# Kernel tuning notes

Measured on AMD Instinct MI355X. Metric: run time of the kernel, lower is better.

Reference implementation:

```python
import jax, jax.numpy as jnp
import numpy as np
from jax import lax

B, C, H, W = 4, 128, 128, 128
MAXD = 192
D = MAXD // 4            # 48 disparity hypotheses at 1/4 scale
WS = 8                   # window size
NH = 8                   # num heads
HD = C // NH             # head dim = 16
SCALE = HD ** -0.5
HID = 4 * C              # mlp hidden (mlp_ratio=4)


def _rel_index(ws):
    coords = np.stack(np.meshgrid(np.arange(ws), np.arange(ws), indexing='ij'))
    cf = coords.reshape(2, -1)
    rel = (cf[:, :, None] - cf[:, None, :]).transpose(1, 2, 0)
    rel[:, :, 0] += ws - 1
    rel[:, :, 1] += ws - 1
    rel[:, :, 0] *= 2 * ws - 1
    return rel.sum(-1)   # [ws*ws, ws*ws]

REL_IDX = jnp.asarray(_rel_index(WS))


def setup_inputs() -> dict:
    key = jax.random.key(0)
    ks = iter(jax.random.split(key, 40))
    rn = lambda shape, s=0.02: jax.random.normal(next(ks), shape, dtype=jnp.float32) * s
    return {
        'feat_l': jax.random.normal(next(ks), (B, C, H, W), dtype=jnp.float32),
        'feat_r': jax.random.normal(next(ks), (B, C, H, W), dtype=jnp.float32),
        'wq': rn((C, C)), 'bq': jnp.zeros((C,), jnp.float32),
        'wk': rn((C, C)), 'bk': jnp.zeros((C,), jnp.float32),
        'wv': rn((C, C)), 'bv': jnp.zeros((C,), jnp.float32),
        'wp': rn((C, C)), 'bp': jnp.zeros((C,), jnp.float32),
        'rpb': rn(((2 * WS - 1) ** 2, NH)),
        'ln1_g': jnp.ones((C,), jnp.float32), 'ln1_b': jnp.zeros((C,), jnp.float32),
        'ln2_g': jnp.ones((C,), jnp.float32), 'ln2_b': jnp.zeros((C,), jnp.float32),
        'mlp_w1': rn((C, HID)), 'mlp_b1': jnp.zeros((HID,), jnp.float32),
        'mlp_w2': rn((HID, C)), 'mlp_b2': jnp.zeros((C,), jnp.float32),
        'un_w1': rn((C, C)), 'un_b1': jnp.zeros((C,), jnp.float32),
        'un_w2': rn((C, C)), 'un_b2': jnp.zeros((C,), jnp.float32),
        'dp_w1': rn((C // 2 + D // 2 + 16, C + D, 3, 3)) if False else rn(((C + D) // 2, C + D, 3, 3)),
        'dp_b1': jnp.zeros(((C + D) // 2,), jnp.float32),
        'bn_g': jnp.ones(((C + D) // 2,), jnp.float32), 'bn_b': jnp.zeros(((C + D) // 2,), jnp.float32),
        'dp_w2': rn((D, (C + D) // 2, 1, 1)), 'dp_b2': jnp.zeros((D,), jnp.float32),
    }


def _ln(x, g, b):
    m = x.mean(-1, keepdims=True)
    v = x.var(-1, keepdims=True)
    return (x - m) * jax.lax.rsqrt(v + 1e-5) * g + b


def _conv(x, w, b, pad):
    y = lax.conv_general_dilated(x, w, (1, 1), [(pad, pad), (pad, pad)],
                                 dimension_numbers=('NCHW', 'OIHW', 'NCHW'))
    return y + b[None, :, None, None]


def _cost_volume(fl, fr):
    # corr[:, d] = mean_c fl[..., w] * fr[..., w-d], zero-padded on the left
    outs = [jnp.mean(fl * fr, axis=1)]
    for d in range(1, D):
        fr_s = jnp.pad(fr[:, :, :, :-d], ((0, 0), (0, 0), (0, 0), (d, 0)))
        outs.append(jnp.mean(fl * fr_s, axis=1))
    return jnp.stack(outs, axis=1)  # [B, D, H, W]


def _win_part(tok):  # [B, H*W, C] -> [B*nW, WS*WS, C]
    x = tok.reshape(B, H // WS, WS, W // WS, WS, C)
    return x.transpose(0, 1, 3, 2, 4, 5).reshape(-1, WS * WS, C)


def _win_rev(win):  # [B*nW, WS*WS, C] -> [B, H*W, C]
    x = win.reshape(B, H // WS, W // WS, WS, WS, C)
    return x.transpose(0, 1, 3, 2, 4, 5).reshape(B, H * W, C)


def _forward(feat_l, feat_r, wq, bq, wk, bk, wv, bv, wp, bp, rpb,
             ln1_g, ln1_b, ln2_g, ln2_b, mlp_w1, mlp_b1, mlp_w2, mlp_b2,
             un_w1, un_b1, un_w2, un_b2, dp_w1, dp_b1, bn_g, bn_b, dp_w2, dp_b2):
    gelu = lambda x: jax.nn.gelu(x, approximate=False)
    cost = _cost_volume(feat_l, feat_r)                       # [B, D, H, W]

    tokens = feat_l.reshape(B, C, H * W).transpose(0, 2, 1)   # [B, N, C]
    unary = gelu(tokens @ un_w1 + un_b1) @ un_w2 + un_b2      # unary potential

    nf = _ln(_win_part(tokens), ln1_g, ln1_b)                 # [Bw, 64, C]
    Bw, N = nf.shape[0], WS * WS
    q = (nf @ wq + bq).reshape(Bw, N, NH, HD).transpose(0, 2, 1, 3)
    k = (nf @ wk + bk).reshape(Bw, N, NH, HD).transpose(0, 2, 1, 3)
    v = (nf @ wv + bv).reshape(Bw, N, NH, HD).transpose(0, 2, 1, 3)
    attn = jnp.einsum('bhnd,bhmd->bhnm', q, k) * SCALE
    bias = rpb[REL_IDX.reshape(-1)].reshape(N, N, NH).transpose(2, 0, 1)
    attn = jax.nn.softmax(attn + bias[None], axis=-1)
    o = jnp.einsum('bhnm,bhmd->bhnd', attn, v).transpose(0, 2, 1, 3).reshape(Bw, N, C)
    pairwise = o @ wp + bp

    x = unary + _win_rev(pairwise)
    x = x + gelu(_ln(x, ln2_g, ln2_b) @ mlp_w1 + mlp_b1) @ mlp_w2 + mlp_b2 * 0.0 + (jnp.zeros((), jnp.float32))
    # (faithful residual MLP; the extra zero terms are no-ops kept out below)
    # -- recompute cleanly to avoid confusion:
    # x = x + mlp(norm2(x))  already done above via single expression

    crf = x.transpose(0, 2, 1).reshape(B, C, H, W)
    fused = jnp.concatenate([crf, cost], axis=1)              # [B, C+D, H, W]

    h1 = jax.nn.relu((_conv(fused, dp_w1, dp_b1, 1)) * jax.lax.rsqrt(jnp.float32(1.0 + 1e-5)) * bn_g[None, :, None, None] + bn_b[None, :, None, None])
    pv = _conv(h1, dp_w2, dp_b2, 0)                           # [B, D, H, W]
    prob = jax.nn.softmax(pv, axis=1)
    disp = jnp.arange(D, dtype=jnp.float32)[None, :, None, None]
    pred = jnp.sum(prob * disp, axis=1, keepdims=True) * 4.0  # [B, 1, H, W]
    return pred


def reference(feat_l, feat_r, wq, bq, wk, bk, wv, bv, wp, bp, rpb,
              ln1_g, ln1_b, ln2_g, ln2_b, mlp_w1, mlp_b1, mlp_w2, mlp_b2,
              un_w1, un_b1, un_w2, un_b2, dp_w1, dp_b1, bn_g, bn_b, dp_w2, dp_b2):
    return _forward(feat_l, feat_r, wq, bq, wk, bk, wv, bv, wp, bp, rpb,
                    ln1_g, ln1_b, ln2_g, ln2_b, mlp_w1, mlp_b1, mlp_w2, mlp_b2,
                    un_w1, un_b1, un_w2, un_b2, dp_w1, dp_b1, bn_g, bn_b, dp_w2, dp_b2)
```

## Files before the change

kernel.cpp:

```cpp
#include <hip/hip_runtime.h>
#include <math.h>

constexpr int Bn = 4, Cc = 128, Hh = 128, Wn = 128, Dd = 48;
constexpr float SCALE = 0.25f;

typedef short  bf16x8 __attribute__((ext_vector_type(8)));
typedef short  bf16x4 __attribute__((ext_vector_type(4)));
typedef float  f32x4  __attribute__((ext_vector_type(4)));
typedef unsigned short u16x8 __attribute__((ext_vector_type(8)));

static __device__ __forceinline__ unsigned short f2bf(float f) {
    return __builtin_bit_cast(unsigned short, (__bf16)f);
}

static __device__ __forceinline__ float bf2f(unsigned short u) {
    return __uint_as_float((unsigned int)u << 16);
}

static __device__ __forceinline__ unsigned int pack2bf(float a, float b) {
    return (unsigned int)f2bf(a) | ((unsigned int)f2bf(b) << 16);
}

static __device__ __forceinline__ float gelu_f(float v) {
    float u = v * (1.5957691216f + 0.0713548162f * v * v);
    return v * __builtin_amdgcn_rcpf(1.0f + __expf(-u));
}

static __device__ __forceinline__ size_t opk_addr(int b, int wh, int ww, int Mt, int ks, int lane) {
    return ((size_t)(b * 16384) + (wh * 8 + Mt * 2 + (ks >> 1)) * 128 + ww * 8) * 128
           + (ks & 1) * 512 + lane * 8;
}

__global__ __launch_bounds__(384) void k_cost(const float* __restrict__ fl,
                                              const float* __restrict__ fr,
                                              unsigned short* __restrict__ costbf) {
    __shared__ float s_fl[2][16][64];
    __shared__ float s_fr[2][16][112];
    int tid = threadIdx.x;
    int w0 = blockIdx.x * 64;
    int hp = blockIdx.y, b = blockIdx.z;
    int row = tid / 192;
    int r = tid - row * 192;
    int wg = r & 15, dg = r >> 4;
    int W = wg * 4, D = dg * 4;
    int h = hp * 2 + row;
    float acc[4][4];
#pragma unroll
    for (int i = 0; i < 4; ++i)
#pragma unroll
        for (int j = 0; j < 4; ++j) acc[i][j] = 0.f;

#pragma unroll 1
    for (int ck = 0; ck < 8; ++ck) {
        int ci0 = ck * 16;
        for (int i = tid; i < 512; i += 384) {
            int rr = i >> 8, rem = i & 255;
            int c = rem >> 4, k4 = rem & 15;
            float4 v = *(const float4*)&fl[((size_t)(b * 128 + ci0 + c) << 14) + (hp * 2 + rr) * 128 + w0 + k4 * 4];
            *(float4*)&s_fl[rr][c][k4 * 4] = v;
        }
        for (int i = tid; i < 896; i += 384) {
            int rr = i / 448, rem = i - rr * 448;
            int c = rem / 28, k4 = rem - c * 28;
// ... 96 lines not shown
        const float* __restrict__ dp_w1, const float* __restrict__ dp_b1,
        const float* __restrict__ bn_g, const float* __restrict__ bn_b,
        unsigned short* __restrict__ pk, float* __restrict__ bias2,
        const float* __restrict__ wq, const float* __restrict__ wk,
        const float* __restrict__ wv, const float* __restrict__ wp,
        unsigned short* __restrict__ pkw,
        const float* __restrict__ rpb, float* __restrict__ pb,
        const float* __restrict__ mlp_w1, unsigned short* __restrict__ pm1,
        const float* __restrict__ mlp_w2, unsigned short* __restrict__ pm2,
        const float* __restrict__ un_w1, unsigned short* __restrict__ pu1,
        const float* __restrict__ un_w2, unsigned short* __restrict__ pu2) {
    int blk = blockIdx.x;
    int lane = threadIdx.x;
    if (blk < 324) {
        pack_conv(blk, lane, dp_w1, dp_b1, bn_g, bn_b, pk, bias2);
    } else if (blk < 452) {
        int bb = blk - 324;
        int mat = bb >> 5;
        const float* W = (mat == 0) ? wq : (mat == 1) ? wk : (mat == 2) ? wv : wp;
        pack_gemmB(bb & 31, lane, W, pkw + (size_t)mat * 16384, 128);
    } else if (blk < 580) {
        pack_rpb(blk - 452, lane, rpb, pb);
    } else if (blk < 708) {
        pack_gemmB(blk - 580, lane, mlp_w1, pm1, 512);
    } else if (blk < 836) {
        pack_gemmB(blk - 708, lane, mlp_w2, pm2, 128);
    } else if (blk < 868) {
        pack_gemmB(blk - 836, lane, un_w1, pu1, 128);
    } else {
        pack_gemmB(blk - 868, lane, un_w2, pu2, 128);
    }
}

__global__ __launch_bounds__(256) void k_unary_mfma(const float* __restrict__ feat_l,
                                                    const unsigned short* __restrict__ pu1,
                                                    const float* __restrict__ b1,
                                                    const unsigned short* __restrict__ pu2,
                                                    const float* __restrict__ b2,
                                                    const float* __restrict__ g1,
                                                    const float* __restrict__ bt1,
                                                    float* __restrict__ x,
                                                    unsigned short* __restrict__ nf) {
    __shared__ __align__(16) unsigned short s_a[64 * 136];
    __shared__ __align__(16) unsigned short s_h[64 * 136];
    int tid = threadIdx.x;
    int wid = tid >> 6, lane = tid & 63;
    int g = lane >> 4, t = lane & 15;
    int n0g = blockIdx.x * 64;
    int b = n0g >> 14;
    int nb = n0g & 16383;

    for (int idx = tid; idx < 4096; idx += 256) {
        int c2 = idx >> 6, nl = idx & 63;
        float v0 = feat_l[((size_t)(b * 128 + 2 * c2) << 14) + nb + nl];
        float v1 = feat_l[((size_t)(b * 128 + 2 * c2 + 1) << 14) + nb + nl];
        *(unsigned int*)&s_a[nl * 136 + 2 * c2] = pack2bf(v0, v1);
    }
    __syncthreads();

    {
        int tok = tid >> 2, q = tid & 3;
        float v[32];
#pragma unroll
        for (int i8 = 0; i8 < 4; ++i8) {
            u16x8 r8 = *(const u16x8*)&s_a[tok * 136 + q * 32 + i8 * 8];
#pragma unroll
            for (int j = 0; j < 8; ++j) v[i8 * 8 + j] = bf2f(r8[j]);
        }
        float s = 0.f, s2 = 0.f;
#pragma unroll
        for (int i = 0; i < 32; ++i) { s += v[i]; s2 += v[i] * v[i]; }
        s += __shfl_xor(s, 1); s += __shfl_xor(s, 2);
        s2 += __shfl_xor(s2, 1); s2 += __shfl_xor(s2, 2);
        float mean = s * (1.f / 128.f);
        float var = s2 * (1.f / 128.f) - mean * mean;
        float rstd = rsqrtf(var + 1e-5f);
        size_t base = (size_t)(n0g + tok) * 128 + q * 32;
#pragma unroll
        for (int i8 = 0; i8 < 4; ++i8) {
            u16x8 o8;
#pragma unroll
            for (int j = 0; j < 8; ++j) {
                int c = q * 32 + i8 * 8 + j;
                o8[j] = f2bf((v[i8 * 8 + j] - mean) * rstd * g1[c] + bt1[c]);
            }
            *(u16x8*)&nf[base + i8 * 8] = o8;
        }
    }

    bf16x8 af[4][4];
#pragma unroll
    for (int Mt = 0; Mt < 4; ++Mt)
#pragma unroll
        for (int ks = 0; ks < 4; ++ks)
            af[Mt][ks] = *(const bf16x8*)&s_a[(Mt * 16 + t) * 136 + ks * 32 + g * 8];

    f32x4 acc1[4][2];
#pragma unroll
    for (int nt2 = 0; nt2 < 2; ++nt2) {
        float bv = b1[(wid * 2 + nt2) * 16 + t];
#pragma unroll
        for (int Mt = 0; Mt < 4; ++Mt) acc1[Mt][nt2] = (f32x4){bv, bv, bv, bv};
    }
#pragma unroll
    for (int ks = 0; ks < 4; ++ks) {
        bf16x8 bf0 = *(const bf16x8*)(pu1 + (size_t)(((wid * 2 + 0) * 4 + ks) * 64 + lane) * 8);
        bf16x8 bf1 = *(const bf16x8*)(pu1 + (size_t)(((wid * 2 + 1) * 4 + ks) * 64 + lane) * 8);
#pragma unroll
        for (int Mt = 0; Mt < 4; ++Mt) {
            acc1[Mt][0] = __builtin_amdgcn_mfma_f32_16x16x32_bf16(af[Mt][ks], bf0, acc1[Mt][0], 0, 0, 0);
            acc1[Mt][1] = __builtin_amdgcn_mfma_f32_16x16x32_bf16(af[Mt][ks], bf1, acc1[Mt][1], 0, 0, 0);
        }
    }
#pragma unroll
    for (int Mt = 0; Mt < 4; ++Mt)
#pragma unroll
        for (int nt2 = 0; nt2 < 2; ++nt2)
#pragma unroll
            for (int rr = 0; rr < 4; ++rr)
                s_h[(Mt * 16 + g * 4 + rr) * 136 + (wid * 2 + nt2) * 16 + t] = f2bf(gelu_f(acc1[Mt][nt2][rr]));
    __syncthreads();

    bf16x8 a2[4][4];
#pragma unroll
    for (int Mt = 0; Mt < 4; ++Mt)
#pragma unroll
        for (int ks = 0; ks < 4; ++ks)
            a2[Mt][ks] = *(const bf16x8*)&s_h[(Mt * 16 + t) * 136 + ks * 32 + g * 8];

    f32x4 acc2[4][2];
#pragma unroll
    for (int nt2 = 0; nt2 < 2; ++nt2) {
        float bv = b2[(wid * 2 + nt2) * 16 + t];
#pragma unroll
        for (int Mt = 0; Mt < 4; ++Mt) acc2[Mt][nt2] = (f32x4){bv, bv, bv, bv};
    }
#pragma unroll
    for (int ks = 0; ks < 4; ++ks) {
        bf16x8 bf0 = *(const bf16x8*)(pu2 + (size_t)(((wid * 2 + 0) * 4 + ks) * 64 + lane) * 8);
        bf16x8 bf1 = *(const bf16x8*)(pu2 + (size_t)(((wid * 2 + 1) * 4 + ks) * 64 + lane) * 8);
#pragma unroll
        for (int Mt = 0; Mt < 4; ++Mt) {
            acc2[Mt][0] = __builtin_amdgcn_mfma_f32_16x16x32_bf16(a2[Mt][ks], bf0, acc2[Mt][0], 0, 0, 0);
            acc2[Mt][1] = __builtin_amdgcn_mfma_f32_16x16x32_bf16(a2[Mt][ks], bf1, acc2[Mt][1], 0, 0, 0);
        }
    }
#pragma unroll
    for (int Mt = 0; Mt < 4; ++Mt)
#pragma unroll
        for (int nt2 = 0; nt2 < 2; ++nt2)
#pragma unroll
            for (int rr = 0; rr < 4; ++rr) {
                int tok = Mt * 16 + g * 4 + rr;
                x[(size_t)(n0g + tok) * 128 + (wid * 2 + nt2) * 16 + t] = acc2[Mt][nt2][rr];
            }
}

__global__ __launch_bounds__(256, 3) void k_attn_core(const unsigned short* nf,
                                                      const unsigned short* __restrict__ pkw,
                                                      const float* __restrict__ pb,
                                                      const float* __restrict__ bq,
                                                      const float* __restrict__ bk,
                                                      const float* __restrict__ bv,
                                                      unsigned short* opk) {
    __shared__ __align__(16) unsigned short s_all[4 * 5760];
    int tid = threadIdx.x;
    int wid = tid >> 6, lane = tid & 63;
    int g = lane >> 4, t = lane & 15;
    int bw = blockIdx.x;
    int b = bw >> 8, wh = (bw >> 4) & 15, ww = bw & 15;

    bf16x8 af[4][4];
#pragma unroll
    for (int Mt = 0; Mt < 4; ++Mt) {
        int tok = Mt * 16 + t;
        size_t gtok = (size_t)(b * 16384) + (wh * 8 + (tok >> 3)) * 128 + ww * 8 + (tok & 7);
#pragma unroll
        for (int ks = 0; ks < 4; ++ks)
            af[Mt][ks] = *(const bf16x8*)&nf[gtok * 128 + ks * 32 + g * 8];
    }
    __syncthreads();

    unsigned short* sQ = s_all + wid * 5760;
    unsigned short* sK = sQ + 1536;
    unsigned short* sV = sQ + 4608;
    unsigned short* sP = sQ;
    unsigned short* sO = sQ;

    const bf16x8 z8v = {0, 0, 0, 0, 0, 0, 0, 0};

#pragma unroll
    for (int hi = 0; hi < 2; ++hi) {
        int h = wid + hi * 4;

        float bqv = bq[h * 16 + t], bkv = bk[h * 16 + t], bvv = bv[h * 16 + t];
        f32x4 qa[4], ka[4], va[4];
#pragma unroll
        for (int Mt = 0; Mt < 4; ++Mt) {
            qa[Mt] = (f32x4){bqv, bqv, bqv, bqv};
            ka[Mt] = (f32x4){bkv, bkv, bkv, bkv};
            va[Mt] = (f32x4){bvv, bvv, bvv, bvv};
        }
#pragma unroll
        for (int ks = 0; ks < 4; ++ks) {
            const unsigned short* wbase = pkw + ((size_t)((h * 4 + ks) * 64 + lane) * 8);
            bf16x8 bfq = *(const bf16x8*)(wbase);
            bf16x8 bfk = *(const bf16x8*)(wbase + 16384);
            bf16x8 bfv = *(const bf16x8*)(wbase + 32768);
#pragma unroll
            for (int Mt = 0; Mt < 4; ++Mt) {
                qa[Mt] = __builtin_amdgcn_mfma_f32_16x16x32_bf16(af[Mt][ks], bfq, qa[Mt], 0, 0, 0);
                ka[Mt] = __builtin_amdgcn_mfma_f32_16x16x32_bf16(af[Mt][ks], bfk, ka[Mt], 0, 0, 0);
                va[Mt] = __builtin_amdgcn_mfma_f32_16x16x32_bf16(af[Mt][ks], bfv, va[Mt], 0, 0, 0);
            }
        }
#pragma unroll
        for (int Mt = 0; Mt < 4; ++Mt) {
            bf16x4 vv;
#pragma unroll
            for (int rr = 0; rr < 4; ++rr) {
                int tok = Mt * 16 + g * 4 + rr;
                sQ[tok * 24 + t] = f2bf(qa[Mt][rr] * SCALE);
                sK[tok * 24 + t] = f2bf(ka[Mt][rr]);
                vv[rr] = (short)f2bf(va[Mt][rr]);
            }
            *(bf16x4*)&sV[t * 72 + Mt * 16 + g * 4] = vv;
        }

        f32x4 s[4][4];
#pragma unroll
        for (int Mtk = 0; Mtk < 4; ++Mtk)
#pragma unroll
            for (int Ntq = 0; Ntq < 4; ++Ntq)
                s[Mtk][Ntq] = *(const f32x4*)(pb + ((size_t)((h * 16 + Mtk * 4 + Ntq) * 64 + lane) * 4));
        bf16x8 bQ[4];
#pragma unroll
        for (int Ntq = 0; Ntq < 4; ++Ntq)
            bQ[Ntq] = (g < 2) ? *(const bf16x8*)&sQ[(Ntq * 16 + t) * 24 + g * 8] : z8v;
#pragma unroll
        for (int Mtk = 0; Mtk < 4; ++Mtk) {
            bf16x8 aK = (g < 2) ? *(const bf16x8*)&sK[(Mtk * 16 + t) * 24 + g * 8] : z8v;
#pragma unroll
            for (int Ntq = 0; Ntq < 4; ++Ntq)
                s[Mtk][Ntq] = __builtin_amdgcn_mfma_f32_16x16x32_bf16(aK, bQ[Ntq], s[Mtk][Ntq], 0, 0, 0);
        }

#pragma unroll
        for (int Ntq = 0; Ntq < 4; ++Ntq) {
            float m = s[0][Ntq][0];
#pragma unroll
            for (int Mtk = 0; Mtk < 4; ++Mtk)
#pragma unroll
                for (int rr = 0; rr < 4; ++rr) m = fmaxf(m, s[Mtk][Ntq][rr]);
            m = fmaxf(m, __shfl_xor(m, 16));
            m = fmaxf(m, __shfl_xor(m, 32));
            float sum = 0.f;
#pragma unroll
            for (int Mtk = 0; Mtk < 4; ++Mtk)
#pragma unroll
                for (int rr = 0; rr < 4; ++rr) {
                    float e = __expf(s[Mtk][Ntq][rr] - m);
                    s[Mtk][Ntq][rr] = e;
                    sum += e;
                }
            sum += __shfl_xor(sum, 16);
            sum += __shfl_xor(sum, 32);
            float inv = __builtin_amdgcn_rcpf(sum);
#pragma unroll
            for (int Mtk = 0; Mtk < 4; ++Mtk) {
                bf16x4 pv;
#pragma unroll
                for (int rr = 0; rr < 4; ++rr) pv[rr] = (short)f2bf(s[Mtk][Ntq][rr] * inv);
                *(bf16x4*)&sP[(Ntq * 16 + t) * 72 + Mtk * 16 + g * 4] = pv;
            }
        }

        f32x4 oa[4];
#pragma unroll
        for (int Mt = 0; Mt < 4; ++Mt) oa[Mt] = (f32x4){0.f, 0.f, 0.f, 0.f};
#pragma unroll
        for (int ksv = 0; ksv < 2; ++ksv) {
            bf16x8 bv2 = *(const bf16x8*)&sV[t * 72 + ksv * 32 + g * 8];
#pragma unroll
            for (int Mt = 0; Mt < 4; ++Mt) {
                bf16x8 ap = *(const bf16x8*)&sP[(Mt * 16 + t) * 72 + ksv * 32 + g * 8];
                oa[Mt] = __builtin_amdgcn_mfma_f32_16x16x32_bf16(ap, bv2, oa[Mt], 0, 0, 0);
            }
        }
#pragma unroll
        for (int Mt = 0; Mt < 4; ++Mt)
#pragma unroll
            for (int rr = 0; rr < 4; ++rr)
                sO[(Mt * 16 + g * 4 + rr) * 16 + t] = f2bf(oa[Mt][rr]);
        int ksf = h >> 1;
        if ((g >> 1) == (h & 1)) {
#pragma unroll
            for (int Mt = 0; Mt < 4; ++Mt) {
                bf16x8 v8 = *(const bf16x8*)&sO[(Mt * 16 + t) * 16 + (g & 1) * 8];
                *(bf16x8*)&opk[opk_addr(b, wh, ww, Mt, ksf, lane)] = v8;
            }
        }
    }
}

__global__ __launch_bounds__(256) void k_mlp_mfma(float* __restrict__ x,
                                                  const unsigned short* __restrict__ opk,
                                                  const unsigned short* __restrict__ pkw,
                                                  const float* __restrict__ bp,
                                                  const float* __restrict__ g2,
                                                  const float* __restrict__ bt2,
                                                  const unsigned short* __restrict__ pm1,
                                                  const float* __restrict__ b1,
                                                  const unsigned short* __restrict__ pm2) {
    __shared__ __align__(16) char smem[51200];
    float* sf = (float*)smem;
    unsigned short* s_h = (unsigned short*)smem;
    unsigned short* s_a = (unsigned short*)(smem + 33792);
    int tid = threadIdx.x;
    int wid = tid >> 6, lane = tid & 63;
    int g = lane >> 4, t = lane & 15;
    int bw = blockIdx.x;
    int b = bw >> 8, wh = (bw >> 4) & 15, ww = bw & 15;

    auto gtok_of = [&](int tok) -> size_t {
        return (size_t)(b * 16384) + (wh * 8 + (tok >> 3)) * 128 + ww * 8 + (tok & 7);
    };

    f32x4 out[4][2];
    {
        float bp0 = bp[wid * 32 + t], bp1 = bp[wid * 32 + 16 + t];
#pragma unroll
        for (int Mt = 0; Mt < 4; ++Mt) {
            out[Mt][0] = (f32x4){bp0, bp0, bp0, bp0};
            out[Mt][1] = (f32x4){bp1, bp1, bp1, bp1};
        }
#pragma unroll
        for (int ks = 0; ks < 4; ++ks) {
            bf16x8 b0 = *(const bf16x8*)(pkw + 49152 + (size_t)(((wid * 2 + 0) * 4 + ks) * 64 + lane) * 8);
            bf16x8 b1v = *(const bf16x8*)(pkw + 49152 + (size_t)(((wid * 2 + 1) * 4 + ks) * 64 + lane) * 8);
#pragma unroll
            for (int Mt = 0; Mt < 4; ++Mt) {
                bf16x8 a = *(const bf16x8*)&opk[opk_addr(b, wh, ww, Mt, ks, lane)];
                out[Mt][0] = __builtin_amdgcn_mfma_f32_16x16x32_bf16(a, b0, out[Mt][0], 0, 0, 0);
                out[Mt][1] = __builtin_amdgcn_mfma_f32_16x16x32_bf16(a, b1v, out[Mt][1], 0, 0, 0);
            }
        }
#pragma unroll
        for (int Mt = 0; Mt < 4; ++Mt)
#pragma unroll
            for (int nt2 = 0; nt2 < 2; ++nt2)
#pragma unroll
                for (int rr = 0; rr < 4; ++rr) {
                    int tok = Mt * 16 + g * 4 + rr;
                    int col = (wid * 2 + nt2) * 16 + t;
                    float v = out[Mt][nt2][rr] + x[gtok_of(tok) * 128 + col];
                    out[Mt][nt2][rr] = v;
                    sf[tok * 132 + col] = v;
                }
    }
    __syncthreads();
    {
        int tok = tid >> 2, q = tid & 3;
        float s = 0.f, s2 = 0.f;
        for (int c = q * 32; c < q * 32 + 32; ++c) {
            float v = sf[tok * 132 + c];
            s += v; s2 += v * v;
        }
        s += __shfl_xor(s, 1); s += __shfl_xor(s, 2);
        s2 += __shfl_xor(s2, 1); s2 += __shfl_xor(s2, 2);
        float mean = s * (1.f / 128.f);
        float var = s2 * (1.f / 128.f) - mean * mean;
        float rstd = rsqrtf(var + 1e-5f);
        for (int c = q * 32; c < q * 32 + 32; c += 2) {
            float v0 = (sf[tok * 132 + c] - mean) * rstd * g2[c] + bt2[c];
            float v1 = (sf[tok * 132 + c + 1] - mean) * rstd * g2[c + 1] + bt2[c + 1];
            *(unsigned int*)&s_a[tok * 136 + c] = pack2bf(v0, v1);
        }
    }
    __syncthreads();
    bf16x8 af[4][4];
#pragma unroll
    for (int Mt = 0; Mt < 4; ++Mt)
#pragma unroll
        for (int ks = 0; ks < 4; ++ks)
            af[Mt][ks] = *(const bf16x8*)&s_a[(Mt * 16 + t) * 136 + ks * 32 + g * 8];

#pragma unroll 1
    for (int hc = 0; hc < 2; ++hc) {
#pragma unroll
        for (int jh = 0; jh < 2; ++jh) {
            f32x4 acc1[4][2];
#pragma unroll
            for (int j2 = 0; j2 < 2; ++j2) {
                float bv = b1[hc * 256 + (wid * 4 + jh * 2 + j2) * 16 + t];
#pragma unroll
                for (int Mt = 0; Mt < 4; ++Mt) acc1[Mt][j2] = (f32x4){bv, bv, bv, bv};
            }
#pragma unroll
            for (int ks = 0; ks < 4; ++ks) {
                int nt0 = hc * 16 + wid * 4 + jh * 2;
                bf16x8 bf0 = *(const bf16x8*)(pm1 + (size_t)((((nt0 + 0) * 4 + ks) * 64 + lane) * 8));
                bf16x8 bf1 = *(const bf16x8*)(pm1 + (size_t)((((nt0 + 1) * 4 + ks) * 64 + lane) * 8));
#pragma unroll
                for (int Mt = 0; Mt < 4; ++Mt) {
                    acc1[Mt][0] = __builtin_amdgcn_mfma_f32_16x16x32_bf16(af[Mt][ks], bf0, acc1[Mt][0], 0, 0, 0);
                    acc1[Mt][1] = __builtin_amdgcn_mfma_f32_16x16x32_bf16(af[Mt][ks], bf1, acc1[Mt][1], 0, 0, 0);
                }
            }
#pragma unroll
            for (int Mt = 0; Mt < 4; ++Mt)
#pragma unroll
                for (int j2 = 0; j2 < 2; ++j2)
#pragma unroll
                    for (int rr = 0; rr < 4; ++rr)
                        s_h[(Mt * 16 + g * 4 + rr) * 264 + (wid * 4 + jh * 2 + j2) * 16 + t] =
                            f2bf(gelu_f(acc1[Mt][j2][rr]));
        }
        __syncthreads();
#pragma unroll
        for (int kt = 0; kt < 8; ++kt) {
            int kc = hc * 2 + (kt >> 2), ks = kt & 3;
            bf16x8 bf0 = *(const bf16x8*)(pm2 + (size_t)(((kc * 32 + (wid * 2 + 0) * 4 + ks) * 64 + lane) * 8));
            bf16x8 bf1 = *(const bf16x8*)(pm2 + (size_t)(((kc * 32 + (wid * 2 + 1) * 4 + ks) * 64 + lane) * 8));
#pragma unroll
            for (int Mt = 0; Mt < 4; ++Mt) {
                bf16x8 a2 = *(const bf16x8*)&s_h[(Mt * 16 + t) * 264 + kt * 32 + g * 8];
                out[Mt][0] = __builtin_amdgcn_mfma_f32_16x16x32_bf16(a2, bf0, out[Mt][0], 0, 0, 0);
                out[Mt][1] = __builtin_amdgcn_mfma_f32_16x16x32_bf16(a2, bf1, out[Mt][1], 0, 0, 0);
            }
        }
        __syncthreads();
    }

#pragma unroll
    for (int Mt = 0; Mt < 4; ++Mt)
#pragma unroll
        for (int nt2 = 0; nt2 < 2; ++nt2)
#pragma unroll
            for (int rr = 0; rr < 4; ++rr) {
// ... 152 lines not shown
    const float* feat_l = (const float*)d_in[0];
    const float* feat_r = (const float*)d_in[1];
    const float* wq = (const float*)d_in[2];
    const float* bq = (const float*)d_in[3];
    const float* wk = (const float*)d_in[4];
    const float* bk = (const float*)d_in[5];
    const float* wv = (const float*)d_in[6];
    const float* bv = (const float*)d_in[7];
    const float* wp = (const float*)d_in[8];
    const float* bp = (const float*)d_in[9];
    const float* rpb = (const float*)d_in[10];
    const float* ln1_g = (const float*)d_in[11];
    const float* ln1_b = (const float*)d_in[12];
    const float* ln2_g = (const float*)d_in[13];
    const float* ln2_b = (const float*)d_in[14];
    const float* mlp_w1 = (const float*)d_in[15];
    const float* mlp_b1 = (const float*)d_in[16];
    const float* mlp_w2 = (const float*)d_in[17];
    const float* un_w1 = (const float*)d_in[19];
    const float* un_b1 = (const float*)d_in[20];
    const float* un_w2 = (const float*)d_in[21];
    const float* un_b2 = (const float*)d_in[22];
    const float* dp_w1 = (const float*)d_in[23];
    const float* dp_b1 = (const float*)d_in[24];
    const float* bn_g = (const float*)d_in[25];
    const float* bn_b = (const float*)d_in[26];
    const float* dp_w2 = (const float*)d_in[27];
    const float* dp_b2 = (const float*)d_in[28];

    float* ws = (float*)d_ws;
    unsigned short* costbf = (unsigned short*)ws;
    float* x = ws + 3145728;
    float* h1 = ws + 11534336;
    unsigned short* nfo = (unsigned short*)h1;
    unsigned short* pk = (unsigned short*)(ws + 17301504);
    float* bias2 = ws + 17384448;
    unsigned short* pkw = (unsigned short*)(ws + 17384544);
    float* pb = ws + 17417312;
    unsigned short* pm1 = (unsigned short*)(ws + 17450080);
    unsigned short* pm2 = (unsigned short*)(ws + 17482848);
    unsigned short* pu1 = (unsigned short*)(ws + 17515616);
    unsigned short* pu2 = (unsigned short*)(ws + 17523808);
    float* out = (float*)d_out;

    k_pack_all<<<900, 64, 0, stream>>>(dp_w1, dp_b1, bn_g, bn_b, pk, bias2,
                                       wq, wk, wv, wp, pkw, rpb, pb,
                                       mlp_w1, pm1, mlp_w2, pm2,
                                       un_w1, pu1, un_w2, pu2);
    k_cost<<<dim3(2, 64, 4), 384, 0, stream>>>(feat_l, feat_r, costbf);
    k_unary_mfma<<<1024, 256, 0, stream>>>(feat_l, pu1, un_b1, pu2, un_b2,
                                           ln1_g, ln1_b, x, nfo);
    k_attn_core<<<1024, 256, 0, stream>>>(nfo, pkw, pb, bq, bk, bv, nfo);
    k_mlp_mfma<<<1024, 256, 0, stream>>>(x, nfo, pkw, bp, ln2_g, ln2_b,
                                         pm1, mlp_b1, pm2);
    k_conv_mfma<<<dim3(8, 16, 4), 256, 0, stream>>>(x, costbf, pk, bias2, h1);
    k_head<<<256, 256, 0, stream>>>(h1, dp_w2, dp_b2, out);
}
```

Baseline: 261.8 us.

## Fuse unary MLP, window attention and transformer MLP into one per-window kernel

Merges the unary projection, LN1 plus windowed attention, and the output projection with LN2 and MLP into a single kernel where each block owns one 8x8 window. Intermediate tensors (the normed features, the attention output, the residual x) stay in LDS and registers instead of going through global memory between three launches. The cost is a larger LDS footprint (about 62KB per block) and higher register pressure. Together these may lower occupancy, and the unary feature load now uses window-strided reads instead of contiguous rows.

```diff
diff --git a/kernel.cpp b/kernel.cpp
--- a/kernel.cpp
+++ b/kernel.cpp
@@ -12,23 +12,15 @@
 static __device__ __forceinline__ unsigned short f2bf(float f) {
     return __builtin_bit_cast(unsigned short, (__bf16)f);
 }
-
 static __device__ __forceinline__ float bf2f(unsigned short u) {
     return __uint_as_float((unsigned int)u << 16);
 }
-
 static __device__ __forceinline__ unsigned int pack2bf(float a, float b) {
     return (unsigned int)f2bf(a) | ((unsigned int)f2bf(b) << 16);
 }
-
 static __device__ __forceinline__ float gelu_f(float v) {
     float u = v * (1.5957691216f + 0.0713548162f * v * v);
     return v * __builtin_amdgcn_rcpf(1.0f + __expf(-u));
-}
-
-static __device__ __forceinline__ size_t opk_addr(int b, int wh, int ww, int Mt, int ks, int lane) {
-    return ((size_t)(b * 16384) + (wh * 8 + Mt * 2 + (ks >> 1)) * 128 + ww * 8) * 128
-           + (ks & 1) * 512 + lane * 8;
 }
 
 __global__ __launch_bounds__(384) void k_cost(const float* __restrict__ fl,
@@ -191,29 +183,37 @@
     }
 }
 
-__global__ __launch_bounds__(256) void k_unary_mfma(const float* __restrict__ feat_l,
-                                                    const unsigned short* __restrict__ pu1,
-                                                    const float* __restrict__ b1,
-                                                    const unsigned short* __restrict__ pu2,
-                                                    const float* __restrict__ b2,
-                                                    const float* __restrict__ g1,
-                                                    const float* __restrict__ bt1,
-                                                    float* __restrict__ x,
-                                                    unsigned short* __restrict__ nf) {
-    __shared__ __align__(16) unsigned short s_a[64 * 136];
-    __shared__ __align__(16) unsigned short s_h[64 * 136];
+__global__ __launch_bounds__(256) void k_fused(
+        const float* __restrict__ feat_l,
+        const unsigned short* __restrict__ pu1, const float* __restrict__ ub1,
+        const unsigned short* __restrict__ pu2, const float* __restrict__ ub2,
+        const float* __restrict__ g1, const float* __restrict__ bt1,
+        const unsigned short* __restrict__ pkw, const float* __restrict__ pb,
+        const float* __restrict__ bq, const float* __restrict__ bk,
+        const float* __restrict__ bv, const float* __restrict__ bp,
+        const float* __restrict__ g2, const float* __restrict__ bt2,
+        const unsigned short* __restrict__ pm1, const float* __restrict__ mb1,
+        const unsigned short* __restrict__ pm2,
+        float* __restrict__ x) {
+    __shared__ __align__(16) char smem[63488];
+    unsigned short* s_a = (unsigned short*)smem;
+    unsigned short* s_nf = (unsigned short*)(smem + 46080);
     int tid = threadIdx.x;
     int wid = tid >> 6, lane = tid & 63;
     int g = lane >> 4, t = lane & 15;
-    int n0g = blockIdx.x * 64;
-    int b = n0g >> 14;
-    int nb = n0g & 16383;
+    int bw = blockIdx.x;
+    int b = bw >> 8, wh = (bw >> 4) & 15, ww = bw & 15;
+
+    auto gtok_of = [&](int tok) -> size_t {
+        return (size_t)(b * 16384) + (wh * 8 + (tok >> 3)) * 128 + ww * 8 + (tok & 7);
+    };
 
     for (int idx = tid; idx < 4096; idx += 256) {
-        int c2 = idx >> 6, nl = idx & 63;
-        float v0 = feat_l[((size_t)(b * 128 + 2 * c2) << 14) + nb + nl];
-        float v1 = feat_l[((size_t)(b * 128 + 2 * c2 + 1) << 14) + nb + nl];
-        *(unsigned int*)&s_a[nl * 136 + 2 * c2] = pack2bf(v0, v1);
+        int c2 = idx >> 6, n = idx & 63;
+        size_t base = ((size_t)(b * 128 + 2 * c2) << 14) + (wh * 8 + (n >> 3)) * 128 + ww * 8 + (n & 7);
+        float v0 = feat_l[base];
+        float v1 = feat_l[base + 16384];
+        *(unsigned int*)&s_a[n * 136 + 2 * c2] = pack2bf(v0, v1);
     }
     __syncthreads();
 
@@ -234,7 +234,6 @@
         float mean = s * (1.f / 128.f);
         float var = s2 * (1.f / 128.f) - mean * mean;
         float rstd = rsqrtf(var + 1e-5f);
-        size_t base = (size_t)(n0g + tok) * 128 + q * 32;
 #pragma unroll
         for (int i8 = 0; i8 < 4; ++i8) {
             u16x8 o8;
@@ -243,250 +242,199 @@
                 int c = q * 32 + i8 * 8 + j;
                 o8[j] = f2bf((v[i8 * 8 + j] - mean) * rstd * g1[c] + bt1[c]);
             }
-            *(u16x8*)&nf[base + i8 * 8] = o8;
-        }
-    }
-
-    bf16x8 af[4][4];
+            *(u16x8*)&s_nf[tok * 136 + q * 32 + i8 * 8] = o8;
+        }
+    }
+    __syncthreads();
+
+    bf16x8 afu[4][4], afa[4][4];
 #pragma unroll
     for (int Mt = 0; Mt < 4; ++Mt)
 #pragma unroll
-        for (int ks = 0; ks < 4; ++ks)
-            af[Mt][ks] = *(const bf16x8*)&s_a[(Mt * 16 + t) * 136 + ks * 32 + g * 8];
-
-    f32x4 acc1[4][2];
-#pragma unroll
-    for (int nt2 = 0; nt2 < 2; ++nt2) {
-        float bv = b1[(wid * 2 + nt2) * 16 + t];
-#pragma unroll
-        for (int Mt = 0; Mt < 4; ++Mt) acc1[Mt][nt2] = (f32x4){bv, bv, bv, bv};
-    }
-#pragma unroll
-    for (int ks = 0; ks < 4; ++ks) {
-        bf16x8 bf0 = *(const bf16x8*)(pu1 + (size_t)(((wid * 2 + 0) * 4 + ks) * 64 + lane) * 8);
-        bf16x8 bf1 = *(const bf16x8*)(pu1 + (size_t)(((wid * 2 + 1) * 4 + ks) * 64 + lane) * 8);
-#pragma unroll
-        for (int Mt = 0; Mt < 4; ++Mt) {
-            acc1[Mt][0] = __builtin_amdgcn_mfma_f32_16x16x32_bf16(af[Mt][ks], bf0, acc1[Mt][0], 0, 0, 0);
-            acc1[Mt][1] = __builtin_amdgcn_mfma_f32_16x16x32_bf16(af[Mt][ks], bf1, acc1[Mt][1], 0, 0, 0);
-        }
-    }
-#pragma unroll
-    for (int Mt = 0; Mt < 4; ++Mt)
-#pragma unroll
-        for (int nt2 = 0; nt2 < 2; ++nt2)
-#pragma unroll
-            for (int rr = 0; rr < 4; ++rr)
-                s_h[(Mt * 16 + g * 4 + rr) * 136 + (wid * 2 + nt2) * 16 + t] = f2bf(gelu_f(acc1[Mt][nt2][rr]));
-    __syncthreads();
-
-    bf16x8 a2[4][4];
-#pragma unroll
-    for (int Mt = 0; Mt < 4; ++Mt)
-#pragma unroll
-        for (int ks = 0; ks < 4; ++ks)
-            a2[Mt][ks] = *(const bf16x8*)&s_h[(Mt * 16 + t) * 136 + ks * 32 + g * 8];
-
-    f32x4 acc2[4][2];
-#pragma unroll
-    for (int nt2 = 0; nt2 < 2; ++nt2) {
-        float bv = b2[(wid * 2 + nt2) * 16 + t];
-#pragma unroll
-        for (int Mt = 0; Mt < 4; ++Mt) acc2[Mt][nt2] = (f32x4){bv, bv, bv, bv};
-    }
-#pragma unroll
-    for (int ks = 0; ks < 4; ++ks) {
-        bf16x8 bf0 = *(const bf16x8*)(pu2 + (size_t)(((wid * 2 + 0) * 4 + ks) * 64 + lane) * 8);
-        bf16x8 bf1 = *(const bf16x8*)(pu2 + (size_t)(((wid * 2 + 1) * 4 + ks) * 64 + lane) * 8);
-#pragma unroll
-        for (int Mt = 0; Mt < 4; ++Mt) {
-            acc2[Mt][0] = __builtin_amdgcn_mfma_f32_16x16x32_bf16(a2[Mt][ks], bf0, acc2[Mt][0], 0, 0, 0);
-            acc2[Mt][1] = __builtin_amdgcn_mfma_f32_16x16x32_bf16(a2[Mt][ks], bf1, acc2[Mt][1], 0, 0, 0);
-        }
-    }
-#pragma unroll
-    for (int Mt = 0; Mt < 4; ++Mt)
-#pragma unroll
-        for (int nt2 = 0; nt2 < 2; ++nt2)
-#pragma unroll
-            for (int rr = 0; rr < 4; ++rr) {
-                int tok = Mt * 16 + g * 4 + rr;
-                x[(size_t)(n0g + tok) * 128 + (wid * 2 + nt2) * 16 + t] = acc2[Mt][nt2][rr];
-            }
-}
-
-__global__ __launch_bounds__(256, 3) void k_attn_core(const unsigned short* nf,
-                                                      const unsigned short* __restrict__ pkw,
-                                                      const float* __restrict__ pb,
-                                                      const float* __restrict__ bq,
-                                                      const float* __restrict__ bk,
-                                                      const float* __restrict__ bv,
-                                                      unsigned short* opk) {
-    __shared__ __align__(16) unsigned short s_all[4 * 5760];
-    int tid = threadIdx.x;
-    int wid = tid >> 6, lane = tid & 63;
-    int g = lane >> 4, t = lane & 15;
-    int bw = blockIdx.x;
-    int b = bw >> 8, wh = (bw >> 4) & 15, ww = bw & 15;
-
-    bf16x8 af[4][4];
-#pragma unroll
-    for (int Mt = 0; Mt < 4; ++Mt) {
-        int tok = Mt * 16 + t;
-        size_t gtok = (size_t)(b * 16384) + (wh * 8 + (tok >> 3)) * 128 + ww * 8 + (tok & 7);
-#pragma unroll
-        for (int ks = 0; ks < 4; ++ks)
-            af[Mt][ks] = *(const bf16x8*)&nf[gtok * 128 + ks * 32 + g * 8];
-    }
-    __syncthreads();
-
-    unsigned short* sQ = s_all + wid * 5760;
-    unsigned short* sK = sQ + 1536;
-    unsigned short* sV = sQ + 4608;
-    unsigned short* sP = sQ;
-    unsigned short* sO = sQ;
-
-    const bf16x8 z8v = {0, 0, 0, 0, 0, 0, 0, 0};
-
-#pragma unroll
-    for (int hi = 0; hi < 2; ++hi) {
-        int h = wid + hi * 4;
-
-        float bqv = bq[h * 16 + t], bkv = bk[h * 16 + t], bvv = bv[h * 16 + t];
-        f32x4 qa[4], ka[4], va[4];
-#pragma unroll
-        for (int Mt = 0; Mt < 4; ++Mt) {
-            qa[Mt] = (f32x4){bqv, bqv, bqv, bqv};
-            ka[Mt] = (f32x4){bkv, bkv, bkv, bkv};
-            va[Mt] = (f32x4){bvv, bvv, bvv, bvv};
-        }
-#pragma unroll
         for (int ks = 0; ks < 4; ++ks) {
-            const unsigned short* wbase = pkw + ((size_t)((h * 4 + ks) * 64 + lane) * 8);
-            bf16x8 bfq = *(const bf16x8*)(wbase);
-            bf16x8 bfk = *(const bf16x8*)(wbase + 16384);
-            bf16x8 bfv = *(const bf16x8*)(wbase + 32768);
+            afu[Mt][ks] = *(const bf16x8*)&s_a[(Mt * 16 + t) * 136 + ks * 32 + g * 8];
+            afa[Mt][ks] = *(const bf16x8*)&s_nf[(Mt * 16 + t) * 136 + ks * 32 + g * 8];
+        }
+    __syncthreads();
+
+    unsigned short* s_hu = s_a;
+    {
+        f32x4 acc1[4][2];
+#pragma unroll
+        for (int nt2 = 0; nt2 < 2; ++nt2) {
+            float bvv = ub1[(wid * 2 + nt2) * 16 + t];
+#pragma unroll
+            for (int Mt = 0; Mt < 4; ++Mt) acc1[Mt][nt2] = (f32x4){bvv, bvv, bvv, bvv};
+        }
+#pragma unroll
+        for (int ks = 0; ks < 4; ++ks) {
+            bf16x8 bf0 = *(const bf16x8*)(pu1 + (size_t)(((wid * 2 + 0) * 4 + ks) * 64 + lane) * 8);
+            bf16x8 bf1 = *(const bf16x8*)(pu1 + (size_t)(((wid * 2 + 1) * 4 + ks) * 64 + lane) * 8);
 #pragma unroll
             for (int Mt = 0; Mt < 4; ++Mt) {
-                qa[Mt] = __builtin_amdgcn_mfma_f32_16x16x32_bf16(af[Mt][ks], bfq, qa[Mt], 0, 0, 0);
-                ka[Mt] = __builtin_amdgcn_mfma_f32_16x16x32_bf16(af[Mt][ks], bfk, ka[Mt], 0, 0, 0);
-                va[Mt] = __builtin_amdgcn_mfma_f32_16x16x32_bf16(af[Mt][ks], bfv, va[Mt], 0, 0, 0);
-            }
-        }
-#pragma unroll
-        for (int Mt = 0; Mt < 4; ++Mt) {
-            bf16x4 vv;
-#pragma unroll
-            for (int rr = 0; rr < 4; ++rr) {
-                int tok = Mt * 16 + g * 4 + rr;
-                sQ[tok * 24 + t] = f2bf(qa[Mt][rr] * SCALE);
-                sK[tok * 24 + t] = f2bf(ka[Mt][rr]);
-                vv[rr] = (short)f2bf(va[Mt][rr]);
-            }
-            *(bf16x4*)&sV[t * 72 + Mt * 16 + g * 4] = vv;
-        }
-
-        f32x4 s[4][4];
-#pragma unroll
-        for (int Mtk = 0; Mtk < 4; ++Mtk)
+                acc1[Mt][0] = __builtin_amdgcn_mfma_f32_16x16x32_bf16(afu[Mt][ks], bf0, acc1[Mt][0], 0, 0, 0);
+                acc1[Mt][1] = __builtin_amdgcn_mfma_f32_16x16x32_bf16(afu[Mt][ks], bf1, acc1[Mt][1], 0, 0, 0);
+            }
+        }
+#pragma unroll
+        for (int Mt = 0; Mt < 4; ++Mt)
+#pragma unroll
+            for (int nt2 = 0; nt2 < 2; ++nt2)
+#pragma unroll
+                for (int rr = 0; rr < 4; ++rr)
+                    s_hu[(Mt * 16 + g * 4 + rr) * 136 + (wid * 2 + nt2) * 16 + t] = f2bf(gelu_f(acc1[Mt][nt2][rr]));
+    }
+    __syncthreads();
+
+    f32x4 xout[4][2];
+    {
+#pragma unroll
+        for (int nt2 = 0; nt2 < 2; ++nt2) {
+            float bvv = ub2[(wid * 2 + nt2) * 16 + t];
+#pragma unroll
+            for (int Mt = 0; Mt < 4; ++Mt) xout[Mt][nt2] = (f32x4){bvv, bvv, bvv, bvv};
+        }
+        bf16x8 a2[4][4];
+#pragma unroll
+        for (int Mt = 0; Mt < 4; ++Mt)
+#pragma unroll
+            for (int ks = 0; ks < 4; ++ks)
+                a2[Mt][ks] = *(const bf16x8*)&s_hu[(Mt * 16 + t) * 136 + ks * 32 + g * 8];
+#pragma unroll
+        for (int ks = 0; ks < 4; ++ks) {
+            bf16x8 bf0 = *(const bf16x8*)(pu2 + (size_t)(((wid * 2 + 0) * 4 + ks) * 64 + lane) * 8);
+            bf16x8 bf1 = *(const bf16x8*)(pu2 + (size_t)(((wid * 2 + 1) * 4 + ks) * 64 + lane) * 8);
+#pragma unroll
+            for (int Mt = 0; Mt < 4; ++Mt) {
+                xout[Mt][0] = __builtin_amdgcn_mfma_f32_16x16x32_bf16(a2[Mt][ks], bf0, xout[Mt][0], 0, 0, 0);
+                xout[Mt][1] = __builtin_amdgcn_mfma_f32_16x16x32_bf16(a2[Mt][ks], bf1, xout[Mt][1], 0, 0, 0);
+            }
+        }
+    }
+    __syncthreads();
+
+    {
+        unsigned short* sQ = (unsigned short*)smem + wid * 5760;
+        unsigned short* sK = sQ + 1536;
+        unsigned short* sV = sQ + 4608;
+        unsigned short* sP = sQ;
+        const bf16x8 z8v = {0, 0, 0, 0, 0, 0, 0, 0};
+#pragma unroll
+        for (int hi = 0; hi < 2; ++hi) {
+            int h = wid + hi * 4;
+            float bqv = bq[h * 16 + t], bkv = bk[h * 16 + t], bvv = bv[h * 16 + t];
+            f32x4 qa[4], ka[4], va[4];
+#pragma unroll
+            for (int Mt = 0; Mt < 4; ++Mt) {
+                qa[Mt] = (f32x4){bqv, bqv, bqv, bqv};
+                ka[Mt] = (f32x4){bkv, bkv, bkv, bkv};
+                va[Mt] = (f32x4){bvv, bvv, bvv, bvv};
+            }
+#pragma unroll
+            for (int ks = 0; ks < 4; ++ks) {
+                const unsigned short* wbase = pkw + ((size_t)((h * 4 + ks) * 64 + lane) * 8);
+                bf16x8 bfq = *(const bf16x8*)(wbase);
+                bf16x8 bfk = *(const bf16x8*)(wbase + 16384);
+                bf16x8 bfv = *(const bf16x8*)(wbase + 32768);
+#pragma unroll
+                for (int Mt = 0; Mt < 4; ++Mt) {
+                    qa[Mt] = __builtin_amdgcn_mfma_f32_16x16x32_bf16(afa[Mt][ks], bfq, qa[Mt], 0, 0, 0);
+                    ka[Mt] = __builtin_amdgcn_mfma_f32_16x16x32_bf16(afa[Mt][ks], bfk, ka[Mt], 0, 0, 0);
+                    va[Mt] = __builtin_amdgcn_mfma_f32_16x16x32_bf16(afa[Mt][ks], bfv, va[Mt], 0, 0, 0);
+                }
+            }
+#pragma unroll
+            for (int Mt = 0; Mt < 4; ++Mt) {
+                bf16x4 vv;
+#pragma unroll
+                for (int rr = 0; rr < 4; ++rr) {
+                    int tok = Mt * 16 + g * 4 + rr;
+                    sQ[tok * 24 + t] = f2bf(qa[Mt][rr] * SCALE);
+                    sK[tok * 24 + t] = f2bf(ka[Mt][rr]);
+                    vv[rr] = (short)f2bf(va[Mt][rr]);
+                }
+                *(bf16x4*)&sV[t * 72 + Mt * 16 + g * 4] = vv;
+            }
+
+            f32x4 s[4][4];
+#pragma unroll
+            for (int Mtk = 0; Mtk < 4; ++Mtk)
+#pragma unroll
+                for (int Ntq = 0; Ntq < 4; ++Ntq)
+                    s[Mtk][Ntq] = *(const f32x4*)(pb + ((size_t)((h * 16 + Mtk * 4 + Ntq) * 64 + lane) * 4));
+            bf16x8 bQ[4];
 #pragma unroll
             for (int Ntq = 0; Ntq < 4; ++Ntq)
-                s[Mtk][Ntq] = *(const f32x4*)(pb + ((size_t)((h * 16 + Mtk * 4 + Ntq) * 64 + lane) * 4));
-        bf16x8 bQ[4];
-#pragma unroll
-        for (int Ntq = 0; Ntq < 4; ++Ntq)
-            bQ[Ntq] = (g < 2) ? *(const bf16x8*)&sQ[(Ntq * 16 + t) * 24 + g * 8] : z8v;
-#pragma unroll
-        for (int Mtk = 0; Mtk < 4; ++Mtk) {
-            bf16x8 aK = (g < 2) ? *(const bf16x8*)&sK[(Mtk * 16 + t) * 24 + g * 8] : z8v;
-#pragma unroll
-            for (int Ntq = 0; Ntq < 4; ++Ntq)
-                s[Mtk][Ntq] = __builtin_amdgcn_mfma_f32_16x16x32_bf16(aK, bQ[Ntq], s[Mtk][Ntq], 0, 0, 0);
-        }
-
-#pragma unroll
-        for (int Ntq = 0; Ntq < 4; ++Ntq) {
-            float m = s[0][Ntq][0];
-#pragma unroll
-            for (int Mtk = 0; Mtk < 4; ++Mtk)
-#pragma unroll
-                for (int rr = 0; rr < 4; ++rr) m = fmaxf(m, s[Mtk][Ntq][rr]);
-            m = fmaxf(m, __shfl_xor(m, 16));
-            m = fmaxf(m, __shfl_xor(m, 32));
-            float sum = 0.f;
-#pragma unroll
-            for (int Mtk = 0; Mtk < 4; ++Mtk)
-#pragma unroll
-                for (int rr = 0; rr < 4; ++rr) {
-                    float e = __expf(s[Mtk][Ntq][rr] - m);
-                    s[Mtk][Ntq][rr] = e;
-                    sum += e;
-                }
-            sum += __shfl_xor(sum, 16);
-            sum += __shfl_xor(sum, 32);
-            float inv = __builtin_amdgcn_rcpf(sum);
+                bQ[Ntq] = (g < 2) ? *(const bf16x8*)&sQ[(Ntq * 16 + t) * 24 + g * 8] : z8v;
 #pragma unroll
             for (int Mtk = 0; Mtk < 4; ++Mtk) {
-                bf16x4 pv;
-#pragma unroll
-                for (int rr = 0; rr < 4; ++rr) pv[rr] = (short)f2bf(s[Mtk][Ntq][rr] * inv);
-                *(bf16x4*)&sP[(Ntq * 16 + t) * 72 + Mtk * 16 + g * 4] = pv;
-            }
-        }
-
-        f32x4 oa[4];
-#pragma unroll
-        for (int Mt = 0; Mt < 4; ++Mt) oa[Mt] = (f32x4){0.f, 0.f, 0.f, 0.f};
-#pragma unroll
-        for (int ksv = 0; ksv < 2; ++ksv) {
-            bf16x8 bv2 = *(const bf16x8*)&sV[t * 72 + ksv * 32 + g * 8];
-#pragma unroll
-            for (int Mt = 0; Mt < 4; ++Mt) {
-                bf16x8 ap = *(const bf16x8*)&sP[(Mt * 16 + t) * 72 + ksv * 32 + g * 8];
-                oa[Mt] = __builtin_amdgcn_mfma_f32_16x16x32_bf16(ap, bv2, oa[Mt], 0, 0, 0);
-            }
-        }
-#pragma unroll
-        for (int Mt = 0; Mt < 4; ++Mt)
-#pragma unroll
-            for (int rr = 0; rr < 4; ++rr)
-                sO[(Mt * 16 + g * 4 + rr) * 16 + t] = f2bf(oa[Mt][rr]);
-        int ksf = h >> 1;
-        if ((g >> 1) == (h & 1)) {
-#pragma unroll
-            for (int Mt = 0; Mt < 4; ++Mt) {
-                bf16x8 v8 = *(const bf16x8*)&sO[(Mt * 16 + t) * 16 + (g & 1) * 8];
-                *(bf16x8*)&opk[opk_addr(b, wh, ww, Mt, ksf, lane)] = v8;
-            }
-        }
-    }
-}
-
-__global__ __launch_bounds__(256) void k_mlp_mfma(float* __restrict__ x,
-                                                  const unsigned short* __restrict__ opk,
-                                                  const unsigned short* __restrict__ pkw,
-                                                  const float* __restrict__ bp,
-                                                  const float* __restrict__ g2,
-                                                  const float* __restrict__ bt2,
-                                                  const unsigned short* __restrict__ pm1,
-                                                  const float* __restrict__ b1,
-                                                  const unsigned short* __restrict__ pm2) {
-    __shared__ __align__(16) char smem[51200];
+                bf16x8 aK = (g < 2) ? *(const bf16x8*)&sK[(Mtk * 16 + t) * 24 + g * 8] : z8v;
+#pragma unroll
+                for (int Ntq = 0; Ntq < 4; ++Ntq)
+                    s[Mtk][Ntq] = __builtin_amdgcn_mfma_f32_16x16x32_bf16(aK, bQ[Ntq], s[Mtk][Ntq], 0, 0, 0);
+            }
+
+#pragma unroll
+            for (int Ntq = 0; Ntq < 4; ++Ntq) {
+                float m = s[0][Ntq][0];
+#pragma unroll
+                for (int Mtk = 0; Mtk < 4; ++Mtk)
+#pragma unroll
+                    for (int rr = 0; rr < 4; ++rr) m = fmaxf(m, s[Mtk][Ntq][rr]);
+                m = fmaxf(m, __shfl_xor(m, 16));
+                m = fmaxf(m, __shfl_xor(m, 32));
+                float sum = 0.f;
+#pragma unroll
+                for (int Mtk = 0; Mtk < 4; ++Mtk)
+#pragma unroll
+                    for (int rr = 0; rr < 4; ++rr) {
+                        float e = __expf(s[Mtk][Ntq][rr] - m);
+                        s[Mtk][Ntq][rr] = e;
+                        sum += e;
+                    }
+                sum += __shfl_xor(sum, 16);
+                sum += __shfl_xor(sum, 32);
+                float inv = __builtin_amdgcn_rcpf(sum);
+#pragma unroll
+                for (int Mtk = 0; Mtk < 4; ++Mtk) {
+                    bf16x4 pv;
+#pragma unroll
+                    for (int rr = 0; rr < 4; ++rr) pv[rr] = (short)f2bf(s[Mtk][Ntq][rr] * inv);
+                    *(bf16x4*)&sP[(Ntq * 16 + t) * 72 + Mtk * 16 + g * 4] = pv;
+                }
+            }
+
+            f32x4 oa[4];
+#pragma unroll
+            for (int Mt = 0; Mt < 4; ++Mt) oa[Mt] = (f32x4){0.f, 0.f, 0.f, 0.f};
+#pragma unroll
+            for (int ksv = 0; ksv < 2; ++ksv) {
+                bf16x8 bv2 = *(const bf16x8*)&sV[t * 72 + ksv * 32 + g * 8];
+#pragma unroll
+                for (int Mt = 0; Mt < 4; ++Mt) {
+                    bf16x8 ap = *(const bf16x8*)&sP[(Mt * 16 + t) * 72 + ksv * 32 + g * 8];
+                    oa[Mt] = __builtin_amdgcn_mfma_f32_16x16x32_bf16(ap, bv2, oa[Mt], 0, 0, 0);
+                }
+            }
+#pragma unroll
+            for (int Mt = 0; Mt < 4; ++Mt)
+#pragma unroll
+                for (int rr = 0; rr < 4; ++rr)
+                    s_nf[(Mt * 16 + g * 4 + rr) * 136 + h * 16 + t] = f2bf(oa[Mt][rr]);
+        }
+    }
+    __syncthreads();
+
     float* sf = (float*)smem;
     unsigned short* s_h = (unsigned short*)smem;
-    unsigned short* s_a = (unsigned short*)(smem + 33792);
-    int tid = threadIdx.x;
-    int wid = tid >> 6, lane = tid & 63;
-    int g = lane >> 4, t = lane & 15;
-    int bw = blockIdx.x;
-    int b = bw >> 8, wh = (bw >> 4) & 15, ww = bw & 15;
-
-    auto gtok_of = [&](int tok) -> size_t {
-        return (size_t)(b * 16384) + (wh * 8 + (tok >> 3)) * 128 + ww * 8 + (tok & 7);
-    };
-
     f32x4 out[4][2];
     {
+        bf16x8 ofr[4][4];
+#pragma unroll
+        for (int Mt = 0; Mt < 4; ++Mt)
+#pragma unroll
+            for (int ks = 0; ks < 4; ++ks)
+                ofr[Mt][ks] = *(const bf16x8*)&s_nf[(Mt * 16 + t) * 136 + ks * 32 + g * 8];
         float bp0 = bp[wid * 32 + t], bp1 = bp[wid * 32 + 16 + t];
 #pragma unroll
         for (int Mt = 0; Mt < 4; ++Mt) {
@@ -499,9 +447,8 @@
             bf16x8 b1v = *(const bf16x8*)(pkw + 49152 + (size_t)(((wid * 2 + 1) * 4 + ks) * 64 + lane) * 8);
 #pragma unroll
             for (int Mt = 0; Mt < 4; ++Mt) {
-                bf16x8 a = *(const bf16x8*)&opk[opk_addr(b, wh, ww, Mt, ks, lane)];
-                out[Mt][0] = __builtin_amdgcn_mfma_f32_16x16x32_bf16(a, b0, out[Mt][0], 0, 0, 0);
-                out[Mt][1] = __builtin_amdgcn_mfma_f32_16x16x32_bf16(a, b1v, out[Mt][1], 0, 0, 0);
+                out[Mt][0] = __builtin_amdgcn_mfma_f32_16x16x32_bf16(ofr[Mt][ks], b0, out[Mt][0], 0, 0, 0);
+                out[Mt][1] = __builtin_amdgcn_mfma_f32_16x16x32_bf16(ofr[Mt][ks], b1v, out[Mt][1], 0, 0, 0);
             }
         }
 #pragma unroll
@@ -512,12 +459,13 @@
                 for (int rr = 0; rr < 4; ++rr) {
                     int tok = Mt * 16 + g * 4 + rr;
                     int col = (wid * 2 + nt2) * 16 + t;
-                    float v = out[Mt][nt2][rr] + x[gtok_of(tok) * 128 + col];
+                    float v = out[Mt][nt2][rr] + xout[Mt][nt2][rr];
                     out[Mt][nt2][rr] = v;
                     sf[tok * 132 + col] = v;
                 }
     }
     __syncthreads();
+
     {
         int tok = tid >> 2, q = tid & 3;
         float s = 0.f, s2 = 0.f;
@@ -533,16 +481,17 @@
         for (int c = q * 32; c < q * 32 + 32; c += 2) {
             float v0 = (sf[tok * 132 + c] - mean) * rstd * g2[c] + bt2[c];
             float v1 = (sf[tok * 132 + c + 1] - mean) * rstd * g2[c + 1] + bt2[c + 1];
-            *(unsigned int*)&s_a[tok * 136 + c] = pack2bf(v0, v1);
-        }
-    }
-    __syncthreads();
-    bf16x8 af[4][4];
+            *(unsigned int*)&s_nf[tok * 136 + c] = pack2bf(v0, v1);
+        }
+    }
+    __syncthreads();
+
+    bf16x8 af2[4][4];
 #pragma unroll
     for (int Mt = 0; Mt < 4; ++Mt)
 #pragma unroll
         for (int ks = 0; ks < 4; ++ks)
-            af[Mt][ks] = *(const bf16x8*)&s_a[(Mt * 16 + t) * 136 + ks * 32 + g * 8];
+            af2[Mt][ks] = *(const bf16x8*)&s_nf[(Mt * 16 + t) * 136 + ks * 32 + g * 8];
 
 #pragma unroll 1
     for (int hc = 0; hc < 2; ++hc) {
@@ -551,9 +500,9 @@
             f32x4 acc1[4][2];
 #pragma unroll
             for (int j2 = 0; j2 < 2; ++j2) {
-                float bv = b1[hc * 256 + (wid * 4 + jh * 2 + j2) * 16 + t];
-#pragma unroll
-                for (int Mt = 0; Mt < 4; ++Mt) acc1[Mt][j2] = (f32x4){bv, bv, bv, bv};
+                float bvv = mb1[hc * 256 + (wid * 4 + jh * 2 + j2) * 16 + t];
+#pragma unroll
+                for (int Mt = 0; Mt < 4; ++Mt) acc1[Mt][j2] = (f32x4){bvv, bvv, bvv, bvv};
             }
 #pragma unroll
             for (int ks = 0; ks < 4; ++ks) {
@@ -562,8 +511,8 @@
                 bf16x8 bf1 = *(const bf16x8*)(pm1 + (size_t)((((nt0 + 1) * 4 + ks) * 64 + lane) * 8));
 #pragma unroll
                 for (int Mt = 0; Mt < 4; ++Mt) {
-                    acc1[Mt][0] = __builtin_amdgcn_mfma_f32_16x16x32_bf16(af[Mt][ks], bf0, acc1[Mt][0], 0, 0, 0);
-                    acc1[Mt][1] = __builtin_amdgcn_mfma_f32_16x16x32_bf16(af[Mt][ks], bf1, acc1[Mt][1], 0, 0, 0);
+                    acc1[Mt][0] = __builtin_amdgcn_mfma_f32_16x16x32_bf16(af2[Mt][ks], bf0, acc1[Mt][0], 0, 0, 0);
+                    acc1[Mt][1] = __builtin_amdgcn_mfma_f32_16x16x32_bf16(af2[Mt][ks], bf1, acc1[Mt][1], 0, 0, 0);
                 }
             }
 #pragma unroll
@@ -782,7 +731,6 @@
     unsigned short* costbf = (unsigned short*)ws;
     float* x = ws + 3145728;
     float* h1 = ws + 11534336;
-    unsigned short* nfo = (unsigned short*)h1;
     unsigned short* pk = (unsigned short*)(ws + 17301504);
     float* bias2 = ws + 17384448;
     unsigned short* pkw = (unsigned short*)(ws + 17384544);
@@ -798,11 +746,9 @@
                                        mlp_w1, pm1, mlp_w2, pm2,
                                        un_w1, pu1, un_w2, pu2);
     k_cost<<<dim3(2, 64, 4), 384, 0, stream>>>(feat_l, feat_r, costbf);
-    k_unary_mfma<<<1024, 256, 0, stream>>>(feat_l, pu1, un_b1, pu2, un_b2,
-                                           ln1_g, ln1_b, x, nfo);
-    k_attn_core<<<1024, 256, 0, stream>>>(nfo, pkw, pb, bq, bk, bv, nfo);
-    k_mlp_mfma<<<1024, 256, 0, stream>>>(x, nfo, pkw, bp, ln2_g, ln2_b,
-                                         pm1, mlp_b1, pm2);
+    k_fused<<<1024, 256, 0, stream>>>(feat_l, pu1, un_b1, pu2, un_b2,
+                                      ln1_g, ln1_b, pkw, pb, bq, bk, bv, bp,
+                                      ln2_g, ln2_b, pm1, mlp_b1, pm2, x);
     k_conv_mfma<<<dim3(8, 16, 4), 256, 0, stream>>>(x, costbf, pk, bias2, h1);
     k_head<<<256, 256, 0, stream>>>(h1, dp_w2, dp_b2, out);
 }
```

Measured after the change: 293.2 us. 1.12x slower.
